# Optimization experiments

Hardware: AMD Instinct MI355X
Metric: run time of the kernel (lower is better)

The kernel has to match this reference:

```python
import jax, jax.numpy as jnp
import numpy as np

B, T, C = 2, 2048, 1024
NH = 16
HD = C // NH

def build_alibi_bias(n_head, max_len):
    slopes = jnp.arange(1, n_head + 1, dtype=jnp.float32) / n_head  # [nh]
    ar = jnp.arange(max_len, dtype=jnp.float32)
    # bias[h, i, j] = slopes[h] * (j - i)
    return slopes[:, None, None] * (ar[None, None, :] - ar[None, :, None])

def setup_inputs() -> dict:
    key = jax.random.key(0)
    ks = jax.random.split(key, 7)
    s = 0.02
    return {
        "x": jax.random.normal(ks[0], (B, T, C), dtype=jnp.float32),
        "q_w": jax.random.normal(ks[1], (C, C), dtype=jnp.float32) * s,   # [in, out]
        "q_b": jnp.zeros((C,), dtype=jnp.float32),
        "kv_w": jax.random.normal(ks[2], (C, 2 * C), dtype=jnp.float32) * s,
        "kv_b": jnp.zeros((2 * C,), dtype=jnp.float32),
        "o_w": jax.random.normal(ks[3], (C, C), dtype=jnp.float32) * s,
        "o_b": jnp.zeros((C,), dtype=jnp.float32),
    }

def reference(x, q_w, q_b, kv_w, kv_b, o_w, o_b):
    Bx, Tx, Cx = x.shape
    q = (x @ q_w + q_b).reshape(Bx, Tx, NH, HD).transpose(0, 2, 1, 3)      # [B,nh,T,hd]
    kv = (x @ kv_w + kv_b).reshape(Bx, Tx, 2, NH, HD).transpose(2, 0, 3, 1, 4)
    k, v = kv[0], kv[1]                                                     # [B,nh,T,hd]
    att = jnp.einsum("bhqd,bhkd->bhqk", q, k) * (1.0 / np.sqrt(HD))        # [B,nh,T,T]
    att = att + build_alibi_bias(NH, Tx)[None]                              # ALiBi bias
    causal = jnp.tril(jnp.ones((Tx, Tx), dtype=bool))
    att = jnp.where(causal[None, None], att, -jnp.inf)
    att = jax.nn.softmax(att, axis=-1)
    y = jnp.einsum("bhqk,bhkd->bhqd", att, v)                               # [B,nh,T,hd]
    y = y.transpose(0, 2, 1, 3).reshape(Bx, Tx, Cx)
    return y @ o_w + o_b
```

## Files before the change

kernel.cpp:

```cpp
#include <hip/hip_runtime.h>
#include <hip/hip_bf16.h>

#define NB 2
#define NT 2048
#define NC 1024
#define NHD 16
#define HDD 64
#define LOG2E 1.4426950408889634f

typedef __attribute__((ext_vector_type(8))) short short8;
typedef __attribute__((ext_vector_type(4))) float f32x4;
typedef __attribute__((ext_vector_type(16))) float f32x16;

__device__ __forceinline__ ushort f2bf(float f) {
    union { float f; unsigned u; } v; v.f = f;
    unsigned u = v.u;
    unsigned r = (u + 0x7FFFu + ((u >> 16) & 1u)) >> 16;
    return (ushort)r;
}

__device__ __forceinline__ float bf2f(ushort u) {
    unsigned x = ((unsigned)u) << 16;
    float f; __builtin_memcpy(&f, &x, 4); return f;
}

__device__ __forceinline__ unsigned pkbf(float a, float b) {
    __hip_bfloat162 t = __float22bfloat162_rn(float2{a, b});
    unsigned u; __builtin_memcpy(&u, &t, 4); return u;
}

__device__ __forceinline__ void gload16(const ushort* g, ushort* l) {
    __builtin_amdgcn_global_load_lds((const __attribute__((address_space(1))) void*)g,
                                     (__attribute__((address_space(3))) void*)l, 16, 0, 0);
}

__device__ __forceinline__ void tcvt_tile(const float* __restrict__ src, ushort* __restrict__ dst,
                                          int Kd, int Nd, int kb, int nb)
{
    __shared__ ushort tile[64][68];
    const int tid = threadIdx.x;
    const int r = tid >> 2, c = (tid & 3) * 16;
    const float* sp = src + (size_t)(kb + r) * Nd + nb + c;
#pragma unroll
    for (int i = 0; i < 16; i += 4) {
        float4 v = *(const float4*)(sp + i);
        tile[r][c + i + 0] = f2bf(v.x);
        tile[r][c + i + 1] = f2bf(v.y);
        tile[r][c + i + 2] = f2bf(v.z);
        tile[r][c + i + 3] = f2bf(v.w);
    }
    __syncthreads();
    ushort* dp = dst + (size_t)(nb + r) * Kd + kb + c;
#pragma unroll
    for (int i = 0; i < 16; i += 8) {
        short8 o;
#pragma unroll
        for (int j = 0; j < 8; j++) o[j] = (short)tile[c + i + j][r];
        *(short8*)(dp + i) = o;
    }
}

__global__ __launch_bounds__(256)
void prep(const float* __restrict__ x, const float* __restrict__ q_w,
          const float* __restrict__ kv_w, const float* __restrict__ o_w,
          ushort* __restrict__ xb, ushort* __restrict__ wqkvT, ushort* __restrict__ woT)
{
    const int bid = blockIdx.x;
    if (bid < 2048) {
        int i = (bid * 256 + threadIdx.x) * 8;
        float4 a = *(const float4*)(x + i);
        float4 b = *(const float4*)(x + i + 4);
        short8 o;
        o[0] = (short)f2bf(a.x); o[1] = (short)f2bf(a.y);
        o[2] = (short)f2bf(a.z); o[3] = (short)f2bf(a.w);
        o[4] = (short)f2bf(b.x); o[5] = (short)f2bf(b.y);
        o[6] = (short)f2bf(b.z); o[7] = (short)f2bf(b.w);
        *(short8*)(xb + i) = o;
    } else if (bid < 2304) {
        int r = bid - 2048;
        tcvt_tile(q_w, wqkvT, 1024, 1024, (r & 15) * 64, (r >> 4) * 64);
    } else if (bid < 2816) {
        int r = bid - 2304;
        tcvt_tile(kv_w, wqkvT + 1024 * 1024, 1024, 2048, (r & 15) * 64, (r >> 4) * 64);
    } else {
        int r = bid - 2816;
        tcvt_tile(o_w, woT, 1024, 1024, (r & 15) * 64, (r >> 4) * 64);
    }
}

__global__ __launch_bounds__(256)
void vtr(const ushort* __restrict__ src, ushort* __restrict__ dst)
{
    __shared__ ushort tile[64][66];
    const int tid = threadIdx.x;
    const int bh = blockIdx.y;
    const int t0 = blockIdx.x * 64;
    const int r = tid >> 2, c = (tid & 3) * 16;
    const ushort* sp = src + ((size_t)bh * NT + t0 + r) * HDD + c;
    *(short8*)&tile[r][c]     = *(const short8*)sp;
    *(short8*)&tile[r][c + 8] = *(const short8*)(sp + 8);
    __syncthreads();
    ushort* dp = dst + ((size_t)bh * HDD + r) * NT + t0 + c;
    short8 o0, o1;
#pragma unroll
    for (int j = 0; j < 8; j++) { o0[j] = (short)tile[c + j][r]; o1[j] = (short)tile[c + 8 + j][r]; }
    *(short8*)dp = o0;
    *(short8*)(dp + 8) = o1;
}

template<int MODE>
__global__ __launch_bounds__(256)
void gemm128(const ushort* __restrict__ A, const ushort* __restrict__ Bt,
             const float* __restrict__ bias0, const float* __restrict__ bias1,
             ushort* __restrict__ Qo, ushort* __restrict__ Ko, ushort* __restrict__ Vo,
             float* __restrict__ Fo, int Kdim)
{
    __shared__ ushort Al[2][128 * 32];
    __shared__ ushort Bl[2][128 * 32];
    const int tid = threadIdx.x;
    const int lane = tid & 63, w = tid >> 6;
    const int wr = (w >> 1) * 64, wc = (w & 1) * 64;
    const int lg = lane >> 4, lc = lane & 15;

    const int nwg = gridDim.x;
    const int cpx = nwg >> 3;
    const int sid = (blockIdx.x & 7) * cpx + (blockIdx.x >> 3);
    const int bm = (sid & 31) * 128, bn = (sid >> 5) * 128;

    f32x4 acc[4][4] = {};

    const int srow = lane >> 2, scol = (lane & 3) * 8;
    const int seg0 = w * 2;

    const ushort* apb = A  + (size_t)(bm + seg0 * 16 + srow) * Kdim + scol;
    const ushort* bpb = Bt + (size_t)(bn + seg0 * 16 + srow) * Kdim + scol;

    gload16(apb,              &Al[0][seg0 * 512]);
    gload16(apb + 16 * Kdim,  &Al[0][(seg0 + 1) * 512]);
    gload16(bpb,              &Bl[0][seg0 * 512]);
    gload16(bpb + 16 * Kdim,  &Bl[0][(seg0 + 1) * 512]);

    int cur = 0;
    for (int k0 = 0; k0 < Kdim; k0 += 32) {
        __syncthreads();
        if (k0 + 32 < Kdim) {
            gload16(apb + (k0 + 32),             &Al[cur ^ 1][seg0 * 512]);
            gload16(apb + (k0 + 32) + 16 * Kdim, &Al[cur ^ 1][(seg0 + 1) * 512]);
            gload16(bpb + (k0 + 32),             &Bl[cur ^ 1][seg0 * 512]);
            gload16(bpb + (k0 + 32) + 16 * Kdim, &Bl[cur ^ 1][(seg0 + 1) * 512]);
        }
        short8 af[4], bfv[4];
#pragma unroll
        for (int mt = 0; mt < 4; mt++) af[mt] = *(const short8*)&Al[cur][(wr + mt*16 + lc) * 32 + lg*8];
#pragma unroll
        for (int nt = 0; nt < 4; nt++) bfv[nt] = *(const short8*)&Bl[cur][(wc + nt*16 + lc) * 32 + lg*8];
        __builtin_amdgcn_s_setprio(1);
#pragma unroll
        for (int mt = 0; mt < 4; mt++)
#pragma unroll
            for (int nt = 0; nt < 4; nt++)
                acc[mt][nt] = __builtin_amdgcn_mfma_f32_16x16x32_bf16(af[mt], bfv[nt], acc[mt][nt], 0, 0, 0);
        __builtin_amdgcn_s_setprio(0);
        cur ^= 1;
    }

#pragma unroll
    for (int mt = 0; mt < 4; mt++) {
#pragma unroll
        for (int nt = 0; nt < 4; nt++) {
#pragma unroll
            for (int rr = 0; rr < 4; rr++) {
                int m = bm + wr + mt*16 + lg*4 + rr;
                int n = bn + wc + nt*16 + lc;
                float v = acc[mt][nt][rr];
                if (MODE == 0) {
                    int b = m >> 11, t = m & 2047;
                    if (n < NC) {
                        float q = (v + bias0[n]) * (0.125f * LOG2E);
                        int hh = n >> 6, d = n & 63;
                        Qo[(((size_t)b*NHD + hh)*NT + t)*HDD + d] = f2bf(q);
                    } else {
                        int j = n - NC;
                        float val = v + bias1[j];
                        int s = j >> 10;
                        int jj = j & 1023;
                        int hh = jj >> 6, d = jj & 63;
                        ushort* dst = s ? Vo : Ko;
                        dst[(((size_t)b*NHD + hh)*NT + t)*HDD + d] = f2bf(val);
                    }
                } else {
                    Fo[(size_t)m * NC + n] = v + bias0[n];
                }
            }
        }
    }
}

__global__ __launch_bounds__(256, 3)
void attn_fwd(const ushort* __restrict__ Q, const ushort* __restrict__ K,
              const ushort* __restrict__ Vt, ushort* __restrict__ Y,
              ushort* __restrict__ pool0, ushort* __restrict__ pool1,
              float* __restrict__ mlb)
{
    __shared__ ushort sb[2 * 2 * 64 * 72];

    const int tid = threadIdx.x;
    const int lane = tid & 63, w = tid >> 6;
    const int lo5 = lane & 31, hi = lane >> 5;
    const int slot = (int)(blockIdx.x >> 5);
    const int bh = blockIdx.x & 31;
    const int b = bh >> 4, h = bh & 15;

    int qt, t_begin, t_end, pi = 0;
    const bool split = (slot < 26);
    if (split) {
        qt = 15 - (slot >> 1);
        const int s = slot & 1;
        t_begin = s * (qt + 1);
        t_end = t_begin + (qt + 1);
        pi = (bh * 13 + (qt - 3)) * 2 + s;
    } else {
        qt = 28 - slot;
        t_begin = 0;
        t_end = 2 * qt + 2;
    }

    const ushort* Qp = Q + (size_t)bh * NT * HDD;
    const ushort* Kp = K + (size_t)bh * NT * HDD;
    const ushort* Vp = Vt + (size_t)bh * HDD * NT;

    const int q0 = qt * 128 + w * 32;
    const int qlane = q0 + lo5;

    const float slope2 = (float)(h + 1) * (LOG2E / (float)NHD);

    short8 qf[4];
    {
        const ushort* qr = Qp + (size_t)qlane * HDD + 8 * hi;
#pragma unroll
        for (int kk = 0; kk < 4; kk++) qf[kk] = *(const short8*)(qr + kk * 16);
    }

    short8 ones;
#pragma unroll
    for (int j = 0; j < 8; j++) ones[j] = (short)0x3F80;

    float bb[16];
#pragma unroll
    for (int r = 0; r < 16; r++) {
        int roff = (r & 3) + 8 * (r >> 2) + 4 * hi;
        bb[r] = slope2 * ((float)roff - (float)qlane);
    }

    float m_s = -1e30f, l_s = 0.f;
    f32x16 accO[2] = {};

    const int sr = tid >> 2, sd = (tid & 3) * 16;

    short8 pk0, pk1, pv0, pv1;
    {
        const ushort* kp = Kp + (size_t)(t_begin * 64 + sr) * HDD + sd;
        pk0 = *(const short8*)kp;
        pk1 = *(const short8*)(kp + 8);
        const ushort* vp = Vp + (size_t)sr * NT + t_begin * 64 + sd;
        pv0 = *(const short8*)vp;
        pv1 = *(const short8*)(vp + 8);
    }

    for (int t = t_begin; t < t_end; t++) {
        const int kv0 = t * 64;
        ushort* Kl = sb + ((t - t_begin) & 1) * 2 * 64 * 72;
        ushort* Vl = Kl + 64 * 72;
        *(short8*)&Kl[sr * 72 + sd]     = pk0;
        *(short8*)&Kl[sr * 72 + sd + 8] = pk1;
        *(short8*)&Vl[sr * 72 + sd]     = pv0;
        *(short8*)&Vl[sr * 72 + sd + 8] = pv1;
        __syncthreads();

        if (t + 1 < t_end) {
            const int kv1 = kv0 + 64;
            const ushort* kp = Kp + (size_t)(kv1 + sr) * HDD + sd;
            pk0 = *(const short8*)kp;
            pk1 = *(const short8*)(kp + 8);
            const ushort* vp = Vp + (size_t)sr * NT + kv1 + sd;
            pv0 = *(const short8*)vp;
            pv1 = *(const short8*)(vp + 8);
        }

#pragma unroll
        for (int sub = 0; sub < 2; sub++) {
            const int kv0s = kv0 + sub * 32;
            if (kv0s > q0 + 31) continue;

            f32x16 S = {};
            __builtin_amdgcn_s_setprio(1);
#pragma unroll
            for (int kk = 0; kk < 4; kk++) {
                short8 kf = *(const short8*)&Kl[(sub * 32 + lo5) * 72 + kk * 16 + 8 * hi];
                S = __builtin_amdgcn_mfma_f32_32x32x16_bf16(kf, qf[kk], S, 0, 0, 0);
            }
            __builtin_amdgcn_s_setprio(0);

            const float sk = slope2 * (float)kv0s;
            float mloc = m_s - sk;

            if (kv0s + 31 > q0) {
#pragma unroll
                for (int r = 0; r < 16; r++) {
                    int kvr = kv0s + (r & 3) + 8 * (r >> 2) + 4 * hi;
                    S[r] = (kvr > qlane) ? -1e30f : (S[r] + bb[r]);
                }
            } else {
#pragma unroll
                for (int r = 0; r < 16; r++) S[r] = S[r] + bb[r];
            }

            float a0 = fmaxf(fmaxf(S[0], S[1]), S[2]);
            float a1 = fmaxf(fmaxf(S[3], S[4]), S[5]);
            float a2 = fmaxf(fmaxf(S[6], S[7]), S[8]);
            float a3 = fmaxf(fmaxf(S[9], S[10]), S[11]);
            float a4 = fmaxf(fmaxf(S[12], S[13]), S[14]);
            float rmax = fmaxf(fmaxf(fmaxf(a0, a1), fmaxf(a2, a3)), fmaxf(a4, S[15]));
            rmax = fmaxf(rmax, __shfl_xor(rmax, 32));

            if (__any(rmax - mloc > 8.0f)) {
                float mn = fmaxf(mloc, rmax);
                float sc = __builtin_amdgcn_exp2f(mloc - mn);
                mloc = mn;
                l_s *= sc;
#pragma unroll
                for (int dt = 0; dt < 2; dt++)
#pragma unroll
                    for (int r = 0; r < 16; r++) accO[dt][r] *= sc;
            }
            m_s = mloc + sk;

#pragma unroll
            for (int r = 0; r < 16; r++)
                S[r] = __builtin_amdgcn_exp2f(S[r] - mloc);

            unsigned pw[8], px[8];
#pragma unroll
            for (int i = 0; i < 8; i++) pw[i] = pkbf(S[2 * i], S[2 * i + 1]);
#pragma unroll
            for (int i = 0; i < 8; i++) px[i] = __shfl_xor(pw[i], 32);
            union { unsigned u[4]; short8 s; } fa0, fa1;
            fa0.u[0] = hi ? px[2] : pw[0];
            fa0.u[1] = hi ? px[3] : pw[1];
            fa0.u[2] = hi ? pw[2] : px[0];
            fa0.u[3] = hi ? pw[3] : px[1];
            fa1.u[0] = hi ? px[6] : pw[4];
            fa1.u[1] = hi ? px[7] : pw[5];
            fa1.u[2] = hi ? pw[6] : px[4];
            fa1.u[3] = hi ? pw[7] : px[5];

            f32x16 z = {};
            __builtin_amdgcn_s_setprio(1);
            z = __builtin_amdgcn_mfma_f32_32x32x16_bf16(ones, fa0.s, z, 0, 0, 0);
            z = __builtin_amdgcn_mfma_f32_32x32x16_bf16(ones, fa1.s, z, 0, 0, 0);

#pragma unroll
            for (int dt = 0; dt < 2; dt++) {
                short8 vf0 = *(const short8*)&Vl[(dt * 32 + lo5) * 72 + sub * 32 + 8 * hi];
                short8 vf1 = *(const short8*)&Vl[(dt * 32 + lo5) * 72 + sub * 32 + 16 + 8 * hi];
                accO[dt] = __builtin_amdgcn_mfma_f32_32x32x16_bf16(vf0, fa0.s, accO[dt], 0, 0, 0);
                accO[dt] = __builtin_amdgcn_mfma_f32_32x32x16_bf16(vf1, fa1.s, accO[dt], 0, 0, 0);
            }
            __builtin_amdgcn_s_setprio(0);

            l_s += z[0];
        }
    }

    const float invl = split ? 1.0f : __builtin_amdgcn_rcpf(l_s);
    __syncthreads();
    ushort* myO = sb + w * 32 * 72;
#pragma unroll
    for (int dt = 0; dt < 2; dt++)
#pragma unroll
        for (int r = 0; r < 16; r++) {
            int d = dt * 32 + (r & 3) + 8 * (r >> 2) + 4 * hi;
            myO[lo5 * 72 + d] = f2bf(accO[dt][r] * invl);
        }
    if (split && hi == 0) {
        int rowin = w * 32 + lo5;
        mlb[pi * 256 + rowin] = m_s;
        mlb[pi * 256 + 128 + rowin] = l_s;
    }
    __syncthreads();
    const int orow = lane >> 1, ocol = (lane & 1) * 32;
    if (split) {
        ushort* pp = (pi < 512 ? pool0 + (size_t)pi * 8192 : pool1 + (size_t)(pi - 512) * 8192)
                     + (w * 32 + orow) * 64 + ocol;
#pragma unroll
        for (int c = 0; c < 4; c++)
            *(short8*)(pp + c * 8) = *(const short8*)&myO[orow * 72 + ocol + c * 8];
    } else {
        ushort* yp = Y + ((size_t)b * NT + q0 + orow) * NC + h * HDD + ocol;
#pragma unroll
        for (int c = 0; c < 4; c++)
            *(short8*)(yp + c * 8) = *(const short8*)&myO[orow * 72 + ocol + c * 8];
    }
}

__global__ __launch_bounds__(256)
void combine(const ushort* __restrict__ pool0, const ushort* __restrict__ pool1,
             const float* __restrict__ mlb, ushort* __restrict__ Y)
{
    const int cb = blockIdx.x;
    const int bh = cb / 13, qs = cb % 13;
    const int qt = qs + 3;
    const int b = bh >> 4, h = bh & 15;
    const int pi0 = (bh * 13 + qs) * 2, pi1 = pi0 + 1;

    const int tid = threadIdx.x;
    const int r = tid >> 1, c0 = (tid & 1) * 32;

    const float m0 = mlb[pi0 * 256 + r], l0 = mlb[pi0 * 256 + 128 + r];
    const float m1 = mlb[pi1 * 256 + r], l1 = mlb[pi1 * 256 + 128 + r];
    const float M = fmaxf(m0, m1);
    const float a0 = __builtin_amdgcn_exp2f(m0 - M);
    const float a1 = __builtin_amdgcn_exp2f(m1 - M);
    const float inv = __builtin_amdgcn_rcpf(a0 * l0 + a1 * l1);

    const ushort* p0 = (pi0 < 512 ? pool0 + (size_t)pi0 * 8192 : pool1 + (size_t)(pi0 - 512) * 8192) + r * 64 + c0;
    const ushort* p1 = (pi1 < 512 ? pool0 + (size_t)pi1 * 8192 : pool1 + (size_t)(pi1 - 512) * 8192) + r * 64 + c0;
    ushort* yp = Y + ((size_t)b * NT + qt * 128 + r) * NC + h * HDD + c0;

#pragma unroll
    for (int c = 0; c < 4; c++) {
        short8 u0 = *(const short8*)(p0 + c * 8);
        short8 u1 = *(const short8*)(p1 + c * 8);
        short8 o;
#pragma unroll
        for (int j = 0; j < 8; j++) {
            float v = (a0 * bf2f((ushort)u0[j]) + a1 * bf2f((ushort)u1[j])) * inv;
            o[j] = (short)f2bf(v);
        }
        *(short8*)(yp + c * 8) = o;
    }
}

extern "C" void kernel_launch(void* const* d_in, const int* in_sizes, int n_in,
                              void* d_out, int out_size, void* d_ws, size_t ws_size,
                              hipStream_t stream)
{
    const float* x    = (const float*)d_in[0];
    const float* q_w  = (const float*)d_in[1];
    const float* q_b  = (const float*)d_in[2];
    const float* kv_w = (const float*)d_in[3];
    const float* kv_b = (const float*)d_in[4];
    const float* o_w  = (const float*)d_in[5];
    const float* o_b  = (const float*)d_in[6];
    float* out = (float*)d_out;

    char* ws = (char*)d_ws;
    ushort* xb    = (ushort*)(ws);
    ushort* wqkvT = (ushort*)(ws + 8388608);
    ushort* woT   = (ushort*)(ws + 14680064);
    ushort* Qs    = (ushort*)(ws + 16777216);
    ushort* Ks    = (ushort*)(ws + 25165824);
    ushort* Vs    = (ushort*)(ws + 33554432);
    ushort* Ys    = (ushort*)(ws + 41943040);
    ushort* VsT   = xb;
    ushort* pool0 = Vs;
    ushort* pool1 = wqkvT;
    float*  mlb   = (float*)(ws + 8388608 + 5242880);

    prep<<<3072, 256, 0, stream>>>(x, q_w, kv_w, o_w, xb, wqkvT, woT);
    gemm128<0><<<768, 256, 0, stream>>>(xb, wqkvT, q_b, kv_b, Qs, Ks, Vs, nullptr, 1024);
    vtr<<<dim3(32,32), 256, 0, stream>>>(Vs, VsT);
    attn_fwd<<<928, 256, 0, stream>>>(Qs, Ks, VsT, Ys, pool0, pool1, mlb);
    combine<<<416, 256, 0, stream>>>(pool0, pool1, mlb, Ys);
    gemm128<1><<<256, 256, 0, stream>>>(Ys, woT, o_b, nullptr, nullptr, nullptr, nullptr, out, 1024);
}
```

Before: 138.6 us.

## Fuse V transpose into QKV GEMM epilogue and rebalance attention split-KV

```diff
diff --git a/kernel.cpp b/kernel.cpp
--- a/kernel.cpp
+++ b/kernel.cpp
@@ -9,6 +9,7 @@
 #define LOG2E 1.4426950408889634f
 
 typedef __attribute__((ext_vector_type(8))) short short8;
+typedef __attribute__((ext_vector_type(4))) short short4v;
 typedef __attribute__((ext_vector_type(4))) float f32x4;
 typedef __attribute__((ext_vector_type(16))) float f32x16;
 
@@ -88,31 +89,11 @@
     }
 }
 
-__global__ __launch_bounds__(256)
-void vtr(const ushort* __restrict__ src, ushort* __restrict__ dst)
-{
-    __shared__ ushort tile[64][66];
-    const int tid = threadIdx.x;
-    const int bh = blockIdx.y;
-    const int t0 = blockIdx.x * 64;
-    const int r = tid >> 2, c = (tid & 3) * 16;
-    const ushort* sp = src + ((size_t)bh * NT + t0 + r) * HDD + c;
-    *(short8*)&tile[r][c]     = *(const short8*)sp;
-    *(short8*)&tile[r][c + 8] = *(const short8*)(sp + 8);
-    __syncthreads();
-    ushort* dp = dst + ((size_t)bh * HDD + r) * NT + t0 + c;
-    short8 o0, o1;
-#pragma unroll
-    for (int j = 0; j < 8; j++) { o0[j] = (short)tile[c + j][r]; o1[j] = (short)tile[c + 8 + j][r]; }
-    *(short8*)dp = o0;
-    *(short8*)(dp + 8) = o1;
-}
-
 template<int MODE>
 __global__ __launch_bounds__(256)
 void gemm128(const ushort* __restrict__ A, const ushort* __restrict__ Bt,
              const float* __restrict__ bias0, const float* __restrict__ bias1,
-             ushort* __restrict__ Qo, ushort* __restrict__ Ko, ushort* __restrict__ Vo,
+             ushort* __restrict__ Qo, ushort* __restrict__ Ko, ushort* __restrict__ VoT,
              float* __restrict__ Fo, int Kdim)
 {
     __shared__ ushort Al[2][128 * 32];
@@ -168,28 +149,37 @@
     for (int mt = 0; mt < 4; mt++) {
 #pragma unroll
         for (int nt = 0; nt < 4; nt++) {
-#pragma unroll
-            for (int rr = 0; rr < 4; rr++) {
-                int m = bm + wr + mt*16 + lg*4 + rr;
-                int n = bn + wc + nt*16 + lc;
-                float v = acc[mt][nt][rr];
-                if (MODE == 0) {
-                    int b = m >> 11, t = m & 2047;
-                    if (n < NC) {
-                        float q = (v + bias0[n]) * (0.125f * LOG2E);
-                        int hh = n >> 6, d = n & 63;
-                        Qo[(((size_t)b*NHD + hh)*NT + t)*HDD + d] = f2bf(q);
-                    } else {
-                        int j = n - NC;
-                        float val = v + bias1[j];
-                        int s = j >> 10;
-                        int jj = j & 1023;
-                        int hh = jj >> 6, d = jj & 63;
-                        ushort* dst = s ? Vo : Ko;
-                        dst[(((size_t)b*NHD + hh)*NT + t)*HDD + d] = f2bf(val);
-                    }
+            const int n = bn + wc + nt * 16 + lc;
+            const int mb = bm + wr + mt * 16 + lg * 4;
+            if (MODE == 1) {
+#pragma unroll
+                for (int rr = 0; rr < 4; rr++)
+                    Fo[(size_t)(mb + rr) * NC + n] = acc[mt][nt][rr] + bias0[n];
+            } else {
+                const int b = mb >> 11, t = mb & 2047;
+                const int reg = n >> 10;
+                if (reg == 0) {
+                    int hh = n >> 6, d = n & 63;
+                    ushort* qp = Qo + (((size_t)b * NHD + hh) * NT + t) * HDD + d;
+#pragma unroll
+                    for (int rr = 0; rr < 4; rr++)
+                        qp[rr * HDD] = f2bf((acc[mt][nt][rr] + bias0[n]) * (0.125f * LOG2E));
+                } else if (reg == 1) {
+                    int j = n - NC;
+                    int hh = j >> 6, d = j & 63;
+                    ushort* kp = Ko + (((size_t)b * NHD + hh) * NT + t) * HDD + d;
+#pragma unroll
+                    for (int rr = 0; rr < 4; rr++)
+                        kp[rr * HDD] = f2bf(acc[mt][nt][rr] + bias1[j]);
                 } else {
-                    Fo[(size_t)m * NC + n] = v + bias0[n];
+                    int j = n - NC;
+                    int jj = j - 1024;
+                    int hh = jj >> 6, d = jj & 63;
+                    short4v o;
+#pragma unroll
+                    for (int rr = 0; rr < 4; rr++)
+                        o[rr] = (short)f2bf(acc[mt][nt][rr] + bias1[j]);
+                    *(short4v*)&VoT[(((size_t)b * NHD + hh) * HDD + d) * NT + t] = o;
                 }
             }
         }
@@ -211,18 +201,19 @@
     const int bh = blockIdx.x & 31;
     const int b = bh >> 4, h = bh & 15;
 
-    int qt, t_begin, t_end, pi = 0;
-    const bool split = (slot < 26);
+    int qt, seg, nseg;
+    if (slot < 16)      { qt = 15 - (slot >> 2); seg = slot & 3; nseg = 4; }
+    else if (slot < 28) { int u = slot - 16; int q3 = u / 3; qt = 11 - q3; seg = u - q3 * 3; nseg = 3; }
+    else if (slot < 36) { int u = slot - 28; qt = 7 - (u >> 1); seg = u & 1; nseg = 2; }
+    else                { qt = 39 - slot; seg = 0; nseg = 1; }
+    const int T = 2 * qt + 2;
+    const int t_begin = (seg * T) / nseg;
+    const int t_end   = ((seg + 1) * T) / nseg;
+    const bool split = (nseg > 1);
+    int pi = 0;
     if (split) {
-        qt = 15 - (slot >> 1);
-        const int s = slot & 1;
-        t_begin = s * (qt + 1);
-        t_end = t_begin + (qt + 1);
-        pi = (bh * 13 + (qt - 3)) * 2 + s;
-    } else {
-        qt = 28 - slot;
-        t_begin = 0;
-        t_end = 2 * qt + 2;
+        int pbase = (qt < 8) ? (qt - 4) * 2 : ((qt < 12) ? 8 + (qt - 8) * 3 : 20 + (qt - 12) * 4);
+        pi = bh * 36 + pbase + seg;
     }
 
     const ushort* Qp = Q + (size_t)bh * NT * HDD;
@@ -390,7 +381,7 @@
     __syncthreads();
     const int orow = lane >> 1, ocol = (lane & 1) * 32;
     if (split) {
-        ushort* pp = (pi < 512 ? pool0 + (size_t)pi * 8192 : pool1 + (size_t)(pi - 512) * 8192)
+        ushort* pp = (pi < 320 ? pool0 + (size_t)pi * 8192 : pool1 + (size_t)(pi - 320) * 8192)
                      + (w * 32 + orow) * 64 + ocol;
 #pragma unroll
         for (int c = 0; c < 4; c++)
@@ -408,35 +399,45 @@
              const float* __restrict__ mlb, ushort* __restrict__ Y)
 {
     const int cb = blockIdx.x;
-    const int bh = cb / 13, qs = cb % 13;
-    const int qt = qs + 3;
+    const int bh = cb / 12, qs = cb % 12;
+    const int qt = qs + 4;
     const int b = bh >> 4, h = bh & 15;
-    const int pi0 = (bh * 13 + qs) * 2, pi1 = pi0 + 1;
+    const int nseg = (qs < 4) ? 2 : ((qs < 8) ? 3 : 4);
+    const int pbase = (qs < 4) ? qs * 2 : ((qs < 8) ? 8 + (qs - 4) * 3 : 20 + (qs - 8) * 4);
+    const int pi0 = bh * 36 + pbase;
 
     const int tid = threadIdx.x;
     const int r = tid >> 1, c0 = (tid & 1) * 32;
 
-    const float m0 = mlb[pi0 * 256 + r], l0 = mlb[pi0 * 256 + 128 + r];
-    const float m1 = mlb[pi1 * 256 + r], l1 = mlb[pi1 * 256 + 128 + r];
-    const float M = fmaxf(m0, m1);
-    const float a0 = __builtin_amdgcn_exp2f(m0 - M);
-    const float a1 = __builtin_amdgcn_exp2f(m1 - M);
-    const float inv = __builtin_amdgcn_rcpf(a0 * l0 + a1 * l1);
-
-    const ushort* p0 = (pi0 < 512 ? pool0 + (size_t)pi0 * 8192 : pool1 + (size_t)(pi0 - 512) * 8192) + r * 64 + c0;
-    const ushort* p1 = (pi1 < 512 ? pool0 + (size_t)pi1 * 8192 : pool1 + (size_t)(pi1 - 512) * 8192) + r * 64 + c0;
+    float m[4], l[4], a[4];
+    float M = -1e30f;
+    for (int s = 0; s < nseg; s++) {
+        m[s] = mlb[(pi0 + s) * 256 + r];
+        l[s] = mlb[(pi0 + s) * 256 + 128 + r];
+        M = fmaxf(M, m[s]);
+    }
+    float L = 0.f;
+    for (int s = 0; s < nseg; s++) { a[s] = __builtin_amdgcn_exp2f(m[s] - M); L += a[s] * l[s]; }
+    const float inv = __builtin_amdgcn_rcpf(L);
+
+    const ushort* pp[4];
+    for (int s = 0; s < nseg; s++) {
+        int pi = pi0 + s;
+        pp[s] = (pi < 320 ? pool0 + (size_t)pi * 8192 : pool1 + (size_t)(pi - 320) * 8192) + r * 64 + c0;
+    }
     ushort* yp = Y + ((size_t)b * NT + qt * 128 + r) * NC + h * HDD + c0;
 
 #pragma unroll
     for (int c = 0; c < 4; c++) {
-        short8 u0 = *(const short8*)(p0 + c * 8);
-        short8 u1 = *(const short8*)(p1 + c * 8);
+        float acc[8] = {};
+        for (int s = 0; s < nseg; s++) {
+            short8 u = *(const short8*)(pp[s] + c * 8);
+#pragma unroll
+            for (int j = 0; j < 8; j++) acc[j] += a[s] * bf2f((ushort)u[j]);
+        }
         short8 o;
 #pragma unroll
-        for (int j = 0; j < 8; j++) {
-            float v = (a0 * bf2f((ushort)u0[j]) + a1 * bf2f((ushort)u1[j])) * inv;
-            o[j] = (short)f2bf(v);
-        }
+        for (int j = 0; j < 8; j++) o[j] = (short)f2bf(acc[j] * inv);
         *(short8*)(yp + c * 8) = o;
     }
 }
@@ -460,17 +461,15 @@
     ushort* woT   = (ushort*)(ws + 14680064);
     ushort* Qs    = (ushort*)(ws + 16777216);
     ushort* Ks    = (ushort*)(ws + 25165824);
-    ushort* Vs    = (ushort*)(ws + 33554432);
+    ushort* VsT   = (ushort*)(ws + 33554432);
     ushort* Ys    = (ushort*)(ws + 41943040);
-    ushort* VsT   = xb;
-    ushort* pool0 = Vs;
-    ushort* pool1 = wqkvT;
-    float*  mlb   = (float*)(ws + 8388608 + 5242880);
+    ushort* pool0 = wqkvT;
+    ushort* pool1 = (ushort*)out;
+    float*  mlb   = (float*)((char*)out + 832 * 16384);
 
     prep<<<3072, 256, 0, stream>>>(x, q_w, kv_w, o_w, xb, wqkvT, woT);
-    gemm128<0><<<768, 256, 0, stream>>>(xb, wqkvT, q_b, kv_b, Qs, Ks, Vs, nullptr, 1024);
-    vtr<<<dim3(32,32), 256, 0, stream>>>(Vs, VsT);
-    attn_fwd<<<928, 256, 0, stream>>>(Qs, Ks, VsT, Ys, pool0, pool1, mlb);
-    combine<<<416, 256, 0, stream>>>(pool0, pool1, mlb, Ys);
+    gemm128<0><<<768, 256, 0, stream>>>(xb, wqkvT, q_b, kv_b, Qs, Ks, VsT, nullptr, 1024);
+    attn_fwd<<<1280, 256, 0, stream>>>(Qs, Ks, VsT, Ys, pool0, pool1, mlb);
+    combine<<<384, 256, 0, stream>>>(pool0, pool1, mlb, Ys);
     gemm128<1><<<256, 256, 0, stream>>>(Ys, woT, o_b, nullptr, nullptr, nullptr, nullptr, out, 1024);
 }
```

New measurement: 132.9 us. -4.1%, faster.
